# Optimization experiments

Hardware: AMD Instinct MI355X
Metric: run time of the kernel (lower is better)

## Reference

```python
import jax, jax.numpy as jnp
import numpy as np

N, E, IN_C, HID_C, OUT_C = 50000, 800000, 64, 64, 8
NEG_SLOPE = 0.2


def setup_inputs() -> dict:
    key = jax.random.key(0)
    ks = jax.random.split(key, 12)
    return {
        "x": jax.random.normal(ks[0], (N, IN_C), dtype=jnp.float32),
        "edge_index": jax.random.randint(ks[1], (2, E), 0, N, dtype=jnp.int64),
        "edge_value": jax.random.uniform(ks[2], (E,), dtype=jnp.float32),
        "W1": jax.random.normal(ks[3], (IN_C, HID_C), dtype=jnp.float32) * 0.1,
        "a1_src": jax.random.normal(ks[4], (HID_C,), dtype=jnp.float32) * 0.1,
        "a1_dst": jax.random.normal(ks[5], (HID_C,), dtype=jnp.float32) * 0.1,
        "b1": jnp.zeros((HID_C,), dtype=jnp.float32),
        "W2": jax.random.normal(ks[6], (HID_C, OUT_C), dtype=jnp.float32) * 0.1,
        "a2_src": jax.random.normal(ks[7], (OUT_C,), dtype=jnp.float32) * 0.1,
        "a2_dst": jax.random.normal(ks[8], (OUT_C,), dtype=jnp.float32) * 0.1,
        "b2": jnp.zeros((OUT_C,), dtype=jnp.float32),
    }


def _rgat_conv(x, src, dst, edge_value, W, a_src, a_dst, b, n_nodes):
    # Linear transform: [N, out_c]
    h = x @ W
    # Per-node attention halves, gathered per edge -> per-edge logit
    e_src = h @ a_src  # [N]
    e_dst = h @ a_dst  # [N]
    logits = jax.nn.leaky_relu(e_src[src] + e_dst[dst], negative_slope=NEG_SLOPE)  # [E]
    # Segment softmax over destination neighborhoods (numerically stable)
    m = jax.ops.segment_max(logits, dst, num_segments=n_nodes)  # [N]
    ex = jnp.exp(logits - m[dst])
    denom = jax.ops.segment_sum(ex, dst, num_segments=n_nodes)  # [N]
    alpha = ex / (denom[dst] + 1e-16)  # [E]
    # Edge-weighted messages, scatter-aggregate to destinations
    msg = (alpha * edge_value)[:, None] * h[src]  # [E, out_c]
    out = jax.ops.segment_sum(msg, dst, num_segments=n_nodes)  # [N, out_c]
    return out + b


def reference(x, edge_index, edge_value, W1, a1_src, a1_dst, b1, W2, a2_src, a2_dst, b2):
    src, dst = edge_index[0], edge_index[1]
    n = x.shape[0]
    hid = _rgat_conv(x, src, dst, edge_value, W1, a1_src, a1_dst, b1, n)
    hid = jax.nn.relu(hid)
    out = _rgat_conv(hid, src, dst, edge_value, W2, a2_src, a2_dst, b2, n)
    return jax.nn.log_softmax(out, axis=1)
```

## Files before the change

### kernel.cpp

```cpp
#include <hip/hip_runtime.h>
#include <hip/hip_fp16.h>
#include <math.h>


#define CHUNK 4096
#define NBKT  256
#define CAP   6144
#define NPW   4

typedef unsigned long long ull;
typedef float v2f __attribute__((ext_vector_type(2)));

struct PartSmem {
    int lhist[NBKT], lbase[NBKT], lcur[NBKT], gbase[NBKT];
    ull buf[CHUNK];
};
struct GemmSmem {
    float4 Wl[64 * 16];
    float  Xt[64 * 64];
};
union FusedSmem { PartSmem p; GemmSmem g; };


__global__ void __launch_bounds__(256) part_gemm_kernel(
    const int* __restrict__ src, const int* __restrict__ dst,
    const float* __restrict__ ev, int* __restrict__ bcnt,
    ull* __restrict__ ped, int E, int nchunks,
    const float* __restrict__ x, const float* __restrict__ W,
    const float* __restrict__ a_src, const float* __restrict__ a_dst,
    unsigned* __restrict__ h, float* __restrict__ es, float* __restrict__ ed,
    int N)
{
    __shared__ FusedSmem sm;
    const int t = threadIdx.x;

    if (blockIdx.x < nchunks) {
        int e0 = blockIdx.x * CHUNK;
        int cnt = min(CHUNK, E - e0);
        sm.p.lhist[t] = 0;
        __syncthreads();
        for (int i = t; i < cnt; i += 256)
            atomicAdd(&sm.p.lhist[dst[e0 + i] >> 8], 1);
        __syncthreads();
        int myc = sm.p.lhist[t];
        sm.p.lbase[t] = myc;
        __syncthreads();
        for (int o = 1; o < 256; o <<= 1) {
            int add = (t >= o) ? sm.p.lbase[t - o] : 0;
            __syncthreads();
            sm.p.lbase[t] += add;
            __syncthreads();
        }
        int excl = sm.p.lbase[t] - myc;
        sm.p.gbase[t] = myc ? atomicAdd(&bcnt[t], myc) : 0;
        __syncthreads();
        sm.p.lbase[t] = excl;
        sm.p.lcur[t] = excl;
        __syncthreads();
        for (int i = t; i < cnt; i += 256) {
            int e = e0 + i;
            int d = dst[e];
            int b = d >> 8;
            unsigned p = (unsigned)src[e] | ((unsigned)(d & 255) << 16)
                       | ((unsigned)b << 24);
            ull q = (ull)p | ((ull)__float_as_uint(ev[e]) << 32);
            int r = atomicAdd(&sm.p.lcur[b], 1);
            sm.p.buf[r] = q;
        }
        __syncthreads();
        for (int i = t; i < cnt; i += 256) {
            ull q = sm.p.buf[i];
            int b = (int)((q >> 24) & 255);
            ped[(size_t)b * CAP + sm.p.gbase[b] + i - sm.p.lbase[b]] = q;
        }
        return;
    }

    const int n0 = (blockIdx.x - nchunks) * 64;

    #pragma unroll
    for (int i = 0; i < 4; ++i)
        sm.g.Wl[t + i * 256] = ((const float4*)W)[t + i * 256];

    #pragma unroll
    for (int i = 0; i < 4; ++i) {
        int f   = t + i * 256;
        int row = f >> 4, kq = f & 15;
        int grow = n0 + row;
        float4 v = make_float4(0.f, 0.f, 0.f, 0.f);
        if (grow < N) v = ((const float4*)x)[(size_t)grow * 16 + kq];
        int rs = row ^ ((kq & 3) << 2);
        sm.g.Xt[(kq * 4 + 0) * 64 + rs] = v.x;
        sm.g.Xt[(kq * 4 + 1) * 64 + rs] = v.y;
        sm.g.Xt[(kq * 4 + 2) * 64 + rs] = v.z;
        sm.g.Xt[(kq * 4 + 3) * 64 + rs] = v.w;
    }

    const int tx = t & 15;
    const int ty = t >> 4;
    const float4 asv = ((const float4*)a_src)[tx];
    const float4 adv = ((const float4*)a_dst)[tx];
    __syncthreads();

    float4 acc0 = make_float4(0.f,0.f,0.f,0.f);
    float4 acc1 = make_float4(0.f,0.f,0.f,0.f);
    float4 acc2 = make_float4(0.f,0.f,0.f,0.f);
    float4 acc3 = make_float4(0.f,0.f,0.f,0.f);

    #pragma unroll 8
    for (int k = 0; k < 64; ++k) {
        int swz = (k >> 2) & 3;
        const float4 xr = *(const float4*)&sm.g.Xt[k * 64 + ((ty ^ swz) << 2)];
        const float4 wv = sm.g.Wl[k * 16 + tx];
        acc0.x += xr.x * wv.x; acc0.y += xr.x * wv.y;
        acc0.z += xr.x * wv.z; acc0.w += xr.x * wv.w;
        acc1.x += xr.y * wv.x; acc1.y += xr.y * wv.y;
        acc1.z += xr.y * wv.z; acc1.w += xr.y * wv.w;
        acc2.x += xr.z * wv.x; acc2.y += xr.z * wv.y;
        acc2.z += xr.z * wv.z; acc2.w += xr.z * wv.w;
        acc3.x += xr.w * wv.x; acc3.y += xr.w * wv.y;
        acc3.z += xr.w * wv.z; acc3.w += xr.w * wv.w;
    }

    float4 accs[4] = {acc0, acc1, acc2, acc3};
    #pragma unroll
    for (int r = 0; r < 4; ++r) {
        int grow = n0 + ty * 4 + r;
        float4 a = accs[r];
        if (grow < N) {
            int lo = __builtin_amdgcn_cvt_pk_fp8_f32(a.x, a.y, 0, false);
            int pk = __builtin_amdgcn_cvt_pk_fp8_f32(a.z, a.w, lo, true);
            h[(size_t)grow * 16 + tx] = (unsigned)pk;
        }
        float ps = a.x * asv.x + a.y * asv.y + a.z * asv.z + a.w * asv.w;
        float pd = a.x * adv.x + a.y * adv.y + a.z * adv.z + a.w * adv.w;
        #pragma unroll
        for (int o = 8; o > 0; o >>= 1) {
            ps += __shfl_xor(ps, o);
            pd += __shfl_xor(pd, o);
        }
        if (tx == 0 && grow < N) { es[grow] = ps; ed[grow] = pd; }
    }
}


__global__ void __launch_bounds__(1024) csr2_kernel(
    const ull* __restrict__ ped, const int* __restrict__ bcnt,
    int* __restrict__ off, int* __restrict__ deg,
    ull* __restrict__ csre, int N)
{
    __shared__ int cl[256], sc[256], cur[256];
    int b = blockIdx.x, t = threadIdx.x;
    const int cnt = min(bcnt[b], CAP);
    const size_t base = (size_t)b * CAP;
    if (t < 256) cl[t] = 0;
    __syncthreads();
    for (int i = t; i < cnt; i += 1024)
        atomicAdd(&cl[(int)((ped[base + i] >> 16) & 255)], 1);
    __syncthreads();
    int myc = (t < 256) ? cl[t] : 0;
    if (t < 256) sc[t] = myc;
    __syncthreads();
    for (int o = 1; o < 256; o <<= 1) {
        int add = (t >= o && t < 256) ? sc[t - o] : 0;
        __syncthreads();
        if (t < 256) sc[t] += add;
        __syncthreads();
    }
    if (t < 256) {
        int excl = sc[t] - myc;
        int node = b * 256 + t;
        if (node < N) { off[node] = (int)base + excl; deg[node] = myc; }
        cur[t] = excl;
    }
    __syncthreads();
    for (int i = t; i < cnt; i += 1024) {
        ull q = ped[base + i];
        int dloc = (int)((q >> 16) & 255);
        int pos = (int)base + atomicAdd(&cur[dloc], 1);
        csre[pos] = (q & 0xFFFFFFFF00000000ull) | (q & 0xFFFFull);
    }
}


__global__ void __launch_bounds__(256) agg64_fused_kernel(
    const int* __restrict__ off, const int* __restrict__ deg,
    const ull* __restrict__ csre,
    const float* __restrict__ es, const float* __restrict__ ed,
    const unsigned* __restrict__ h, const float* __restrict__ b1,
    const float* __restrict__ W2, const float* __restrict__ a2s,
    const float* __restrict__ a2d, float* __restrict__ h2,
    float* __restrict__ es2, float* __restrict__ ed2, int N)
{
    const int wid = threadIdx.x >> 6, lane = threadIdx.x & 63;
    const int g  = lane >> 4;
    const int c4 = lane & 15;
    const int n0 = (blockIdx.x * 4 + wid) * NPW;
    if (n0 >= N) return;
    const int n1 = min(n0 + NPW, N);

    const int c0 = 2 * g, c1 = 2 * g + 1;
    float w2r0[4], w2r1[4];
    #pragma unroll
    for (int j = 0; j < 4; ++j) {
        w2r0[j] = W2[(4 * c4 + j) * 8 + c0];
        w2r1[j] = W2[(4 * c4 + j) * 8 + c1];
    }
    const float4 b1v = *(const float4*)&b1[c4 << 2];
    const float a2sv0 = a2s[c0], a2sv1 = a2s[c1];
    const float a2dv0 = a2d[c0], a2dv1 = a2d[c1];

    int offv = 0, degv = 0;
    float edv = 0.f;
    {
        int nn = n0 + (lane & (NPW - 1));
        if (nn < N) { offv = off[nn]; degv = deg[nn]; edv = ed[nn]; }
    }

    int svS; float evS, esS;
    unsigned pu0, pu1, pu2, pu3;
    {
        int begX = __shfl(offv, 0);
        int cntX = min(__shfl(degv, 0), 64);
        int idxX = begX + min(lane, max(cntX, 1) - 1);
        ull recX = csre[idxX];
        svS = (int)(recX & 0xFFFFull);
        evS = __uint_as_float((unsigned)(recX >> 32));
        esS = es[svS];
        int s0 = __shfl(svS, g),     s1 = __shfl(svS, 4 + g);
        int s2 = __shfl(svS, 8 + g), s3 = __shfl(svS, 12 + g);
        pu0 = h[(size_t)s0 * 16 + c4];
        pu1 = h[(size_t)s1 * 16 + c4];
        pu2 = h[(size_t)s2 * 16 + c4];
        pu3 = h[(size_t)s3 * 16 + c4];
    }

    for (int n = n0; n < n1; ++n) {
        const int nl = n - n0;
        const int beg = __shfl(offv, nl);
        const int dg  = __shfl(degv, nl);
        const float edn = __shfl(edv, nl);
        const int cnt0 = min(dg, 64);

        const int   sv = svS;
        float z = esS + edn;
        float l = z > 0.f ? z : 0.2f * z;
        float q = (lane < cnt0) ? __expf(l) : 0.f;
        float den = q;
        const float wv = q * evS;

        const unsigned cu0 = pu0, cu1 = pu1, cu2 = pu2, cu3 = pu3;

        if (n + 1 < n1) {
            int begX = __shfl(offv, nl + 1);
            int cntX = min(__shfl(degv, nl + 1), 64);
            int idxX = begX + min(lane, max(cntX, 1) - 1);
            ull recX = csre[idxX];
            svS = (int)(recX & 0xFFFFull);
            evS = __uint_as_float((unsigned)(recX >> 32));
            esS = es[svS];
            int s0 = __shfl(svS, g),     s1 = __shfl(svS, 4 + g);
            int s2 = __shfl(svS, 8 + g), s3 = __shfl(svS, 12 + g);
            pu0 = h[(size_t)s0 * 16 + c4];
            pu1 = h[(size_t)s1 * 16 + c4];
            pu2 = h[(size_t)s2 * 16 + c4];
            pu3 = h[(size_t)s3 * 16 + c4];
        }

        float4 acc = make_float4(0.f, 0.f, 0.f, 0.f);
        {
            float w0 = __shfl(wv, g),     w1 = __shfl(wv, 4 + g);
            float w2 = __shfl(wv, 8 + g), w3 = __shfl(wv, 12 + g);
            v2f f0a = __builtin_amdgcn_cvt_pk_f32_fp8((int)cu0, false);
            v2f f0b = __builtin_amdgcn_cvt_pk_f32_fp8((int)cu0, true);
            v2f f1a = __builtin_amdgcn_cvt_pk_f32_fp8((int)cu1, false);
            v2f f1b = __builtin_amdgcn_cvt_pk_f32_fp8((int)cu1, true);
            v2f f2a = __builtin_amdgcn_cvt_pk_f32_fp8((int)cu2, false);
            v2f f2b = __builtin_amdgcn_cvt_pk_f32_fp8((int)cu2, true);
            v2f f3a = __builtin_amdgcn_cvt_pk_f32_fp8((int)cu3, false);
            v2f f3b = __builtin_amdgcn_cvt_pk_f32_fp8((int)cu3, true);
            acc.x += w0 * f0a.x + w1 * f1a.x + w2 * f2a.x + w3 * f3a.x;
            acc.y += w0 * f0a.y + w1 * f1a.y + w2 * f2a.y + w3 * f3a.y;
            acc.z += w0 * f0b.x + w1 * f1b.x + w2 * f2b.x + w3 * f3b.x;
            acc.w += w0 * f0b.y + w1 * f1b.y + w2 * f2b.y + w3 * f3b.y;
        }
        for (int j = 16; j < cnt0; j += 16) {
            int j0 = j + g, j1 = j + 4 + g, j2 = j + 8 + g, j3 = j + 12 + g;
            int   s0 = __shfl(sv, j0), s1 = __shfl(sv, j1);
            int   s2 = __shfl(sv, j2), s3 = __shfl(sv, j3);
            float w0 = __shfl(wv, j0), w1 = __shfl(wv, j1);
            float w2 = __shfl(wv, j2), w3 = __shfl(wv, j3);
            const unsigned u0 = h[(size_t)s0 * 16 + c4];
            const unsigned u1 = h[(size_t)s1 * 16 + c4];
            const unsigned u2 = h[(size_t)s2 * 16 + c4];
            const unsigned u3 = h[(size_t)s3 * 16 + c4];
            v2f f0a = __builtin_amdgcn_cvt_pk_f32_fp8((int)u0, false);
            v2f f0b = __builtin_amdgcn_cvt_pk_f32_fp8((int)u0, true);
            v2f f1a = __builtin_amdgcn_cvt_pk_f32_fp8((int)u1, false);
            v2f f1b = __builtin_amdgcn_cvt_pk_f32_fp8((int)u1, true);
            v2f f2a = __builtin_amdgcn_cvt_pk_f32_fp8((int)u2, false);
            v2f f2b = __builtin_amdgcn_cvt_pk_f32_fp8((int)u2, true);
            v2f f3a = __builtin_amdgcn_cvt_pk_f32_fp8((int)u3, false);
            v2f f3b = __builtin_amdgcn_cvt_pk_f32_fp8((int)u3, true);
            acc.x += w0 * f0a.x + w1 * f1a.x + w2 * f2a.x + w3 * f3a.x;
            acc.y += w0 * f0a.y + w1 * f1a.y + w2 * f2a.y + w3 * f3a.y;
            acc.z += w0 * f0b.x + w1 * f1b.x + w2 * f2b.x + w3 * f3b.x;
            acc.w += w0 * f0b.y + w1 * f1b.y + w2 * f2b.y + w3 * f3b.y;
        }
        for (int base = beg + 64; base < beg + dg; base += 64) {
            const int cnt = min(beg + dg - base, 64);
            const int idx = base + min(lane, cnt - 1);
            const ull rec = csre[idx];
            const int sv2 = (int)(rec & 0xFFFFull);
            const float ev2 = __uint_as_float((unsigned)(rec >> 32));
            float z2 = es[sv2] + edn;
            float l2 = z2 > 0.f ? z2 : 0.2f * z2;
            float q2 = (lane < cnt) ? __expf(l2) : 0.f;
            den += q2;
            const float wv2 = q2 * ev2;
            for (int j = 0; j < cnt; j += 16) {
                int j0 = j + g, j1 = j + 4 + g, j2 = j + 8 + g, j3 = j + 12 + g;
                int   s0 = __shfl(sv2, j0), s1 = __shfl(sv2, j1);
                int   s2 = __shfl(sv2, j2), s3 = __shfl(sv2, j3);
                float w0 = __shfl(wv2, j0), w1 = __shfl(wv2, j1);
                float w2 = __shfl(wv2, j2), w3 = __shfl(wv2, j3);
                const unsigned u0 = h[(size_t)s0 * 16 + c4];
                const unsigned u1 = h[(size_t)s1 * 16 + c4];
                const unsigned u2 = h[(size_t)s2 * 16 + c4];
                const unsigned u3 = h[(size_t)s3 * 16 + c4];
                v2f f0a = __builtin_amdgcn_cvt_pk_f32_fp8((int)u0, false);
                v2f f0b = __builtin_amdgcn_cvt_pk_f32_fp8((int)u0, true);
                v2f f1a = __builtin_amdgcn_cvt_pk_f32_fp8((int)u1, false);
                v2f f1b = __builtin_amdgcn_cvt_pk_f32_fp8((int)u1, true);
                v2f f2a = __builtin_amdgcn_cvt_pk_f32_fp8((int)u2, false);
                v2f f2b = __builtin_amdgcn_cvt_pk_f32_fp8((int)u2, true);
                v2f f3a = __builtin_amdgcn_cvt_pk_f32_fp8((int)u3, false);
                v2f f3b = __builtin_amdgcn_cvt_pk_f32_fp8((int)u3, true);
                acc.x += w0 * f0a.x + w1 * f1a.x + w2 * f2a.x + w3 * f3a.x;
                acc.y += w0 * f0a.y + w1 * f1a.y + w2 * f2a.y + w3 * f3a.y;
                acc.z += w0 * f0b.x + w1 * f1b.x + w2 * f2b.x + w3 * f3b.x;
                acc.w += w0 * f0b.y + w1 * f1b.y + w2 * f2b.y + w3 * f3b.y;
            }
        }

        #pragma unroll
        for (int o = 16; o < 64; o <<= 1) {
            acc.x += __shfl_xor(acc.x, o);
            acc.y += __shfl_xor(acc.y, o);
            acc.z += __shfl_xor(acc.z, o);
            acc.w += __shfl_xor(acc.w, o);
        }
        #pragma unroll
        for (int o = 1; o < 64; o <<= 1) den += __shfl_xor(den, o);

        const float inv = 1.f / (den + 1e-16f);
        float4 hid;
        hid.x = fmaxf(acc.x * inv + b1v.x, 0.f);
        hid.y = fmaxf(acc.y * inv + b1v.y, 0.f);
        hid.z = fmaxf(acc.z * inv + b1v.z, 0.f);
        hid.w = fmaxf(acc.w * inv + b1v.w, 0.f);

        float p0 = hid.x * w2r0[0] + hid.y * w2r0[1] + hid.z * w2r0[2] + hid.w * w2r0[3];
        float p1 = hid.x * w2r1[0] + hid.y * w2r1[1] + hid.z * w2r1[2] + hid.w * w2r1[3];
        #pragma unroll
        for (int o = 1; o < 16; o <<= 1) {
            p0 += __shfl_xor(p0, o);
            p1 += __shfl_xor(p1, o);
        }
        float psv = p0 * a2sv0 + p1 * a2sv1;
        float pdv = p0 * a2dv0 + p1 * a2dv1;
        #pragma unroll
        for (int o = 16; o < 64; o <<= 1) {
            psv += __shfl_xor(psv, o);
            pdv += __shfl_xor(pdv, o);
        }
        if (c4 == 0)
            *(float2*)&h2[(size_t)n * 8 + c0] = make_float2(p0, p1);
        if (lane == 0) { es2[n] = psv; ed2[n] = pdv; }
    }
}


__global__ void __launch_bounds__(256) agg8_lsm_kernel(
    const int* __restrict__ off, const int* __restrict__ deg,
    const ull* __restrict__ csre,
    const float* __restrict__ es, const float* __restrict__ ed,
    const float* __restrict__ h2, const float* __restrict__ b,
    float* __restrict__ out, int N)
{
    const int wid = threadIdx.x >> 6, lane = threadIdx.x & 63;
    const int g  = lane >> 2;
    const int cp = lane & 3;
    const int n0 = (blockIdx.x * 4 + wid) * NPW;
    if (n0 >= N) return;
    const int n1 = min(n0 + NPW, N);
    const float bc0 = b[2 * cp], bc1 = b[2 * cp + 1];

    int offv = 0, degv = 0;
    float edv = 0.f;
    {
        int nn = n0 + (lane & (NPW - 1));
        if (nn < N) { offv = off[nn]; degv = deg[nn]; edv = ed[nn]; }
    }

    int svS; float evS, esS;
    float2 pf0, pf1;
    {
        int begX = __shfl(offv, 0);
        int cntX = min(__shfl(degv, 0), 64);
        int idxX = begX + min(lane, max(cntX, 1) - 1);
        ull recX = csre[idxX];
        svS = (int)(recX & 0xFFFFull);
        evS = __uint_as_float((unsigned)(recX >> 32));
        esS = es[svS];
        int s0 = __shfl(svS, g), s1 = __shfl(svS, 16 + g);
        pf0 = *(const float2*)&h2[(size_t)s0 * 8 + 2 * cp];
        pf1 = *(const float2*)&h2[(size_t)s1 * 8 + 2 * cp];
    }

    for (int n = n0; n < n1; ++n) {
        const int nl = n - n0;
        const int beg = __shfl(offv, nl);
        const int dg  = __shfl(degv, nl);
        const float edn = __shfl(edv, nl);
        const int cnt0 = min(dg, 64);

        const int   sv = svS;
        float z = esS + edn;
        float l = z > 0.f ? z : 0.2f * z;
        float q = (lane < cnt0) ? __expf(l) : 0.f;
        float den = q;
        const float wv = q * evS;

        const float2 cf0 = pf0, cf1 = pf1;

        if (n + 1 < n1) {
            int begX = __shfl(offv, nl + 1);
            int cntX = min(__shfl(degv, nl + 1), 64);
            int idxX = begX + min(lane, max(cntX, 1) - 1);
            ull recX = csre[idxX];
            svS = (int)(recX & 0xFFFFull);
            evS = __uint_as_float((unsigned)(recX >> 32));
            esS = es[svS];
            int s0 = __shfl(svS, g), s1 = __shfl(svS, 16 + g);
            pf0 = *(const float2*)&h2[(size_t)s0 * 8 + 2 * cp];
            pf1 = *(const float2*)&h2[(size_t)s1 * 8 + 2 * cp];
        }

        float a0, a1;
        {
            float w0 = __shfl(wv, g), w1 = __shfl(wv, 16 + g);
            a0 = w0 * cf0.x + w1 * cf1.x;
            a1 = w0 * cf0.y + w1 * cf1.y;
        }
        for (int j = 32; j < cnt0; j += 32) {
            int j0 = j + g, j1 = j + 16 + g;
            int   s0 = __shfl(sv, j0), s1 = __shfl(sv, j1);
            float w0 = __shfl(wv, j0), w1 = __shfl(wv, j1);
            const float2 f0 = *(const float2*)&h2[(size_t)s0 * 8 + 2 * cp];
            const float2 f1 = *(const float2*)&h2[(size_t)s1 * 8 + 2 * cp];
            a0 += w0 * f0.x + w1 * f1.x;
            a1 += w0 * f0.y + w1 * f1.y;
        }
        for (int base = beg + 64; base < beg + dg; base += 64) {
            const int cnt = min(beg + dg - base, 64);
            const int idx = base + min(lane, cnt - 1);
            const ull rec = csre[idx];
            const int sv2 = (int)(rec & 0xFFFFull);
            const float ev2 = __uint_as_float((unsigned)(rec >> 32));
            float z2 = es[sv2] + edn;
            float l2 = z2 > 0.f ? z2 : 0.2f * z2;
            float q2 = (lane < cnt) ? __expf(l2) : 0.f;
            den += q2;
            const float wv2 = q2 * ev2;
            for (int j = 0; j < cnt; j += 32) {
                int j0 = j + g, j1 = j + 16 + g;
                int   s0 = __shfl(sv2, j0), s1 = __shfl(sv2, j1);
                float w0 = __shfl(wv2, j0), w1 = __shfl(wv2, j1);
                const float2 f0 = *(const float2*)&h2[(size_t)s0 * 8 + 2 * cp];
                const float2 f1 = *(const float2*)&h2[(size_t)s1 * 8 + 2 * cp];
                a0 += w0 * f0.x + w1 * f1.x;
                a1 += w0 * f0.y + w1 * f1.y;
            }
        }

        #pragma unroll
        for (int o = 4; o < 64; o <<= 1) {
            a0 += __shfl_xor(a0, o);
            a1 += __shfl_xor(a1, o);
        }
        #pragma unroll
        for (int o = 1; o < 64; o <<= 1) den += __shfl_xor(den, o);

        const float inv = 1.f / (den + 1e-16f);
        float v0 = a0 * inv + bc0;
        float v1 = a1 * inv + bc1;
        float vm = fmaxf(v0, v1);
        vm = fmaxf(vm, __shfl_xor(vm, 1));
        vm = fmaxf(vm, __shfl_xor(vm, 2));
        float s = __expf(v0 - vm) + __expf(v1 - vm);
        s += __shfl_xor(s, 1);
        s += __shfl_xor(s, 2);
        float lse = vm + logf(s);
        if (lane < 4)
            *(float2*)&out[(size_t)n * 8 + 2 * cp] = make_float2(v0 - lse, v1 - lse);
    }
}


extern "C" void kernel_launch(void* const* d_in, const int* in_sizes, int n_in,
                              void* d_out, int out_size, void* d_ws, size_t ws_size,
                              hipStream_t stream)
{
    const float* x   = (const float*)d_in[0];
    const int*   ei  = (const int*)d_in[1];
    const float* ev  = (const float*)d_in[2];
    const float* W1  = (const float*)d_in[3];
    const float* a1s = (const float*)d_in[4];
    const float* a1d = (const float*)d_in[5];
    const float* b1  = (const float*)d_in[6];
    const float* W2  = (const float*)d_in[7];
    const float* a2s = (const float*)d_in[8];
    const float* a2d = (const float*)d_in[9];
    const float* b2  = (const float*)d_in[10];
    float* out = (float*)d_out;

    const int N = in_sizes[0] / 64;
    const int E = in_sizes[2];
    const int* srcp = ei;
    const int* dstp = ei + E;
    const int nchunks = (E + CHUNK - 1) / CHUNK;
    const int ngemm   = (N + 63) / 64;
    const int nbuck = (N + 255) / 256;
    const int nodes_per_block = 4 * NPW;

    ull*   ped  = (ull*)d_ws;
    ull*   csre = ped + (size_t)NBKT * CAP;
    int*   bcnt = (int*)(csre + (size_t)NBKT * CAP);
    int*   off  = bcnt + NBKT;
    int*   deg  = off + N;
    float* es1  = (float*)(deg + N);
    float* ed1  = es1 + N;
    float* es2  = ed1 + N;
    float* ed2  = es2 + N;
    unsigned* h1 = (unsigned*)(ed2 + N);
    float* h2   = (float*)(h1 + (size_t)N * 16);

    hipMemsetAsync(bcnt, 0, NBKT * sizeof(int), stream);

    part_gemm_kernel<<<nchunks + ngemm, 256, 0, stream>>>(
        srcp, dstp, ev, bcnt, ped, E, nchunks,
        x, W1, a1s, a1d, h1, es1, ed1, N);

    csr2_kernel<<<nbuck, 1024, 0, stream>>>(ped, bcnt, off, deg, csre, N);

    agg64_fused_kernel<<<(N + nodes_per_block - 1) / nodes_per_block, 256, 0, stream>>>(
        off, deg, csre, es1, ed1, h1, b1, W2, a2s, a2d, h2, es2, ed2, N);

    agg8_lsm_kernel<<<(N + nodes_per_block - 1) / nodes_per_block, 256, 0, stream>>>(
        off, deg, csre, es2, ed2, h2, b2, out, N);
}
```

Measured before the change: 157.1 us.

## Widen per-lane gathers and use transpose-reduce butterflies in aggregation kernels

Both aggregation kernels now assign fewer edges per lane group but load wider vectors per lane (uint4 of fp8 in layer one, float4 in layer two), so each lane issues one wide gather per edge instead of several narrow ones. Cross-lane reduction switches to a halving transpose-reduce butterfly, where lanes exchange half their partial vector at each step and end up owning a single channel. The fused W2 projection and the log-softmax are reworked around that per-lane channel ownership. This cuts the number of memory instructions and shuffles, at the cost of more accumulator registers (16 floats per lane in layer one) and more select logic in the reductions.

New measurement: 156.6 us. No clear change (-0.3%).

```diff
diff --git a/kernel.cpp b/kernel.cpp
--- a/kernel.cpp
+++ b/kernel.cpp
@@ -183,6 +183,26 @@
 }
 
 
+#define UNPACK_ACC16(u, we)                                              \
+    do {                                                                 \
+        v2f f0a = __builtin_amdgcn_cvt_pk_f32_fp8((int)(u).x, false);    \
+        v2f f0b = __builtin_amdgcn_cvt_pk_f32_fp8((int)(u).x, true);     \
+        v2f f1a = __builtin_amdgcn_cvt_pk_f32_fp8((int)(u).y, false);    \
+        v2f f1b = __builtin_amdgcn_cvt_pk_f32_fp8((int)(u).y, true);     \
+        v2f f2a = __builtin_amdgcn_cvt_pk_f32_fp8((int)(u).z, false);    \
+        v2f f2b = __builtin_amdgcn_cvt_pk_f32_fp8((int)(u).z, true);     \
+        v2f f3a = __builtin_amdgcn_cvt_pk_f32_fp8((int)(u).w, false);    \
+        v2f f3b = __builtin_amdgcn_cvt_pk_f32_fp8((int)(u).w, true);     \
+        acc[0]  += (we) * f0a.x;  acc[1]  += (we) * f0a.y;               \
+        acc[2]  += (we) * f0b.x;  acc[3]  += (we) * f0b.y;               \
+        acc[4]  += (we) * f1a.x;  acc[5]  += (we) * f1a.y;               \
+        acc[6]  += (we) * f1b.x;  acc[7]  += (we) * f1b.y;               \
+        acc[8]  += (we) * f2a.x;  acc[9]  += (we) * f2a.y;               \
+        acc[10] += (we) * f2b.x;  acc[11] += (we) * f2b.y;               \
+        acc[12] += (we) * f3a.x;  acc[13] += (we) * f3a.y;               \
+        acc[14] += (we) * f3b.x;  acc[15] += (we) * f3b.y;               \
+    } while (0)
+
 __global__ void __launch_bounds__(256) agg64_fused_kernel(
     const int* __restrict__ off, const int* __restrict__ deg,
     const ull* __restrict__ csre,
@@ -193,22 +213,24 @@
     float* __restrict__ es2, float* __restrict__ ed2, int N)
 {
     const int wid = threadIdx.x >> 6, lane = threadIdx.x & 63;
-    const int g  = lane >> 4;
-    const int c4 = lane & 15;
+    const int eslot = lane >> 2;
+    const int q     = lane & 3;
     const int n0 = (blockIdx.x * 4 + wid) * NPW;
     if (n0 >= N) return;
     const int n1 = min(n0 + NPW, N);
 
-    const int c0 = 2 * g, c1 = 2 * g + 1;
-    float w2r0[4], w2r1[4];
-    #pragma unroll
-    for (int j = 0; j < 4; ++j) {
-        w2r0[j] = W2[(4 * c4 + j) * 8 + c0];
-        w2r1[j] = W2[(4 * c4 + j) * 8 + c1];
-    }
-    const float4 b1v = *(const float4*)&b1[c4 << 2];
-    const float a2sv0 = a2s[c0], a2sv1 = a2s[c1];
-    const float a2dv0 = a2d[c0], a2dv1 = a2d[c1];
+    const int ch = 16 * q + 8 * ((lane >> 2) & 1) + 4 * ((lane >> 3) & 1)
+                 + 2 * ((lane >> 4) & 1) + ((lane >> 5) & 1);
+    const float b1c = b1[ch];
+    float w2row[8];
+    {
+        const float4 wa = ((const float4*)(W2 + ch * 8))[0];
+        const float4 wb = ((const float4*)(W2 + ch * 8))[1];
+        w2row[0] = wa.x; w2row[1] = wa.y; w2row[2] = wa.z; w2row[3] = wa.w;
+        w2row[4] = wb.x; w2row[5] = wb.y; w2row[6] = wb.z; w2row[7] = wb.w;
+    }
+    const int olane = 4 * (lane & 1) + 2 * ((lane >> 1) & 1) + ((lane >> 2) & 1);
+    const float a2sv = a2s[olane], a2dv = a2d[olane];
 
     int offv = 0, degv = 0;
     float edv = 0.f;
@@ -218,7 +240,7 @@
     }
 
     int svS; float evS, esS;
-    unsigned pu0, pu1, pu2, pu3;
+    uint4 puS;
     {
         int begX = __shfl(offv, 0);
         int cntX = min(__shfl(degv, 0), 64);
@@ -227,12 +249,8 @@
         svS = (int)(recX & 0xFFFFull);
         evS = __uint_as_float((unsigned)(recX >> 32));
         esS = es[svS];
-        int s0 = __shfl(svS, g),     s1 = __shfl(svS, 4 + g);
-        int s2 = __shfl(svS, 8 + g), s3 = __shfl(svS, 12 + g);
-        pu0 = h[(size_t)s0 * 16 + c4];
-        pu1 = h[(size_t)s1 * 16 + c4];
-        pu2 = h[(size_t)s2 * 16 + c4];
-        pu3 = h[(size_t)s3 * 16 + c4];
+        int s0 = __shfl(svS, eslot);
+        puS = *(const uint4*)&h[(size_t)s0 * 16 + q * 4];
     }
 
     for (int n = n0; n < n1; ++n) {
@@ -242,14 +260,14 @@
         const float edn = __shfl(edv, nl);
         const int cnt0 = min(dg, 64);
 
-        const int   sv = svS;
+        const int sv = svS;
         float z = esS + edn;
         float l = z > 0.f ? z : 0.2f * z;
-        float q = (lane < cnt0) ? __expf(l) : 0.f;
-        float den = q;
-        const float wv = q * evS;
-
-        const unsigned cu0 = pu0, cu1 = pu1, cu2 = pu2, cu3 = pu3;
+        float qv = (lane < cnt0) ? __expf(l) : 0.f;
+        float den = qv;
+        const float wv = qv * evS;
+
+        const uint4 cu = puS;
 
         if (n + 1 < n1) {
             int begX = __shfl(offv, nl + 1);
@@ -259,57 +277,27 @@
             svS = (int)(recX & 0xFFFFull);
             evS = __uint_as_float((unsigned)(recX >> 32));
             esS = es[svS];
-            int s0 = __shfl(svS, g),     s1 = __shfl(svS, 4 + g);
-            int s2 = __shfl(svS, 8 + g), s3 = __shfl(svS, 12 + g);
-            pu0 = h[(size_t)s0 * 16 + c4];
-            pu1 = h[(size_t)s1 * 16 + c4];
-            pu2 = h[(size_t)s2 * 16 + c4];
-            pu3 = h[(size_t)s3 * 16 + c4];
-        }
-
-        float4 acc = make_float4(0.f, 0.f, 0.f, 0.f);
-        {
-            float w0 = __shfl(wv, g),     w1 = __shfl(wv, 4 + g);
-            float w2 = __shfl(wv, 8 + g), w3 = __shfl(wv, 12 + g);
-            v2f f0a = __builtin_amdgcn_cvt_pk_f32_fp8((int)cu0, false);
-            v2f f0b = __builtin_amdgcn_cvt_pk_f32_fp8((int)cu0, true);
-            v2f f1a = __builtin_amdgcn_cvt_pk_f32_fp8((int)cu1, false);
-            v2f f1b = __builtin_amdgcn_cvt_pk_f32_fp8((int)cu1, true);
-            v2f f2a = __builtin_amdgcn_cvt_pk_f32_fp8((int)cu2, false);
-            v2f f2b = __builtin_amdgcn_cvt_pk_f32_fp8((int)cu2, true);
-            v2f f3a = __builtin_amdgcn_cvt_pk_f32_fp8((int)cu3, false);
-            v2f f3b = __builtin_amdgcn_cvt_pk_f32_fp8((int)cu3, true);
-            acc.x += w0 * f0a.x + w1 * f1a.x + w2 * f2a.x + w3 * f3a.x;
-            acc.y += w0 * f0a.y + w1 * f1a.y + w2 * f2a.y + w3 * f3a.y;
-            acc.z += w0 * f0b.x + w1 * f1b.x + w2 * f2b.x + w3 * f3b.x;
-            acc.w += w0 * f0b.y + w1 * f1b.y + w2 * f2b.y + w3 * f3b.y;
+            int s0 = __shfl(svS, eslot);
+            puS = *(const uint4*)&h[(size_t)s0 * 16 + q * 4];
+        }
+
+        float acc[16];
+        #pragma unroll
+        for (int k = 0; k < 16; ++k) acc[k] = 0.f;
+
+        {
+            float we = __shfl(wv, eslot);
+            UNPACK_ACC16(cu, we);
         }
         for (int j = 16; j < cnt0; j += 16) {
-            int j0 = j + g, j1 = j + 4 + g, j2 = j + 8 + g, j3 = j + 12 + g;
-            int   s0 = __shfl(sv, j0), s1 = __shfl(sv, j1);
-            int   s2 = __shfl(sv, j2), s3 = __shfl(sv, j3);
-            float w0 = __shfl(wv, j0), w1 = __shfl(wv, j1);
-            float w2 = __shfl(wv, j2), w3 = __shfl(wv, j3);
-            const unsigned u0 = h[(size_t)s0 * 16 + c4];
-            const unsigned u1 = h[(size_t)s1 * 16 + c4];
-            const unsigned u2 = h[(size_t)s2 * 16 + c4];
-            const unsigned u3 = h[(size_t)s3 * 16 + c4];
-            v2f f0a = __builtin_amdgcn_cvt_pk_f32_fp8((int)u0, false);
-            v2f f0b = __builtin_amdgcn_cvt_pk_f32_fp8((int)u0, true);
-            v2f f1a = __builtin_amdgcn_cvt_pk_f32_fp8((int)u1, false);
-            v2f f1b = __builtin_amdgcn_cvt_pk_f32_fp8((int)u1, true);
-            v2f f2a = __builtin_amdgcn_cvt_pk_f32_fp8((int)u2, false);
-            v2f f2b = __builtin_amdgcn_cvt_pk_f32_fp8((int)u2, true);
-            v2f f3a = __builtin_amdgcn_cvt_pk_f32_fp8((int)u3, false);
-            v2f f3b = __builtin_amdgcn_cvt_pk_f32_fp8((int)u3, true);
-            acc.x += w0 * f0a.x + w1 * f1a.x + w2 * f2a.x + w3 * f3a.x;
-            acc.y += w0 * f0a.y + w1 * f1a.y + w2 * f2a.y + w3 * f3a.y;
-            acc.z += w0 * f0b.x + w1 * f1b.x + w2 * f2b.x + w3 * f3b.x;
-            acc.w += w0 * f0b.y + w1 * f1b.y + w2 * f2b.y + w3 * f3b.y;
-        }
-        for (int base = beg + 64; base < beg + dg; base += 64) {
-            const int cnt = min(beg + dg - base, 64);
-            const int idx = base + min(lane, cnt - 1);
+            int   se = __shfl(sv, j + eslot);
+            float we = __shfl(wv, j + eslot);
+            const uint4 u = *(const uint4*)&h[(size_t)se * 16 + q * 4];
+            UNPACK_ACC16(u, we);
+        }
+        for (int base2 = beg + 64; base2 < beg + dg; base2 += 64) {
+            const int cnt = min(beg + dg - base2, 64);
+            const int idx = base2 + min(lane, cnt - 1);
             const ull rec = csre[idx];
             const int sv2 = (int)(rec & 0xFFFFull);
             const float ev2 = __uint_as_float((unsigned)(rec >> 32));
@@ -319,64 +307,101 @@
             den += q2;
             const float wv2 = q2 * ev2;
             for (int j = 0; j < cnt; j += 16) {
-                int j0 = j + g, j1 = j + 4 + g, j2 = j + 8 + g, j3 = j + 12 + g;
-                int   s0 = __shfl(sv2, j0), s1 = __shfl(sv2, j1);
-                int   s2 = __shfl(sv2, j2), s3 = __shfl(sv2, j3);
-                float w0 = __shfl(wv2, j0), w1 = __shfl(wv2, j1);
-                float w2 = __shfl(wv2, j2), w3 = __shfl(wv2, j3);
-                const unsigned u0 = h[(size_t)s0 * 16 + c4];
-                const unsigned u1 = h[(size_t)s1 * 16 + c4];
-                const unsigned u2 = h[(size_t)s2 * 16 + c4];
-                const unsigned u3 = h[(size_t)s3 * 16 + c4];
-                v2f f0a = __builtin_amdgcn_cvt_pk_f32_fp8((int)u0, false);
-                v2f f0b = __builtin_amdgcn_cvt_pk_f32_fp8((int)u0, true);
-                v2f f1a = __builtin_amdgcn_cvt_pk_f32_fp8((int)u1, false);
-                v2f f1b = __builtin_amdgcn_cvt_pk_f32_fp8((int)u1, true);
-                v2f f2a = __builtin_amdgcn_cvt_pk_f32_fp8((int)u2, false);
-                v2f f2b = __builtin_amdgcn_cvt_pk_f32_fp8((int)u2, true);
-                v2f f3a = __builtin_amdgcn_cvt_pk_f32_fp8((int)u3, false);
-                v2f f3b = __builtin_amdgcn_cvt_pk_f32_fp8((int)u3, true);
-                acc.x += w0 * f0a.x + w1 * f1a.x + w2 * f2a.x + w3 * f3a.x;
-                acc.y += w0 * f0a.y + w1 * f1a.y + w2 * f2a.y + w3 * f3a.y;
-                acc.z += w0 * f0b.x + w1 * f1b.x + w2 * f2b.x + w3 * f3b.x;
-                acc.w += w0 * f0b.y + w1 * f1b.y + w2 * f2b.y + w3 * f3b.y;
-            }
-        }
-
+                int   se = __shfl(sv2, j + eslot);
+                float we = __shfl(wv2, j + eslot);
+                const uint4 u = *(const uint4*)&h[(size_t)se * 16 + q * 4];
+                UNPACK_ACC16(u, we);
+            }
+        }
+
+        float r8[8];
+        {
+            const bool hi = (lane & 4);
+            #pragma unroll
+            for (int k = 0; k < 8; ++k) {
+                float keep = hi ? acc[k + 8] : acc[k];
+                float send = hi ? acc[k]     : acc[k + 8];
+                r8[k] = keep + __shfl_xor(send, 4);
+            }
+            den += __shfl_xor(den, 4);
+        }
+        float r4[4];
+        {
+            const bool hi = (lane & 8);
+            #pragma unroll
+            for (int k = 0; k < 4; ++k) {
+                float keep = hi ? r8[k + 4] : r8[k];
+                float send = hi ? r8[k]     : r8[k + 4];
+                r4[k] = keep + __shfl_xor(send, 8);
+            }
+            den += __shfl_xor(den, 8);
+        }
+        float r2[2];
+        {
+            const bool hi = (lane & 16);
+            #pragma unroll
+            for (int k = 0; k < 2; ++k) {
+                float keep = hi ? r4[k + 2] : r4[k];
+                float send = hi ? r4[k]     : r4[k + 2];
+                r2[k] = keep + __shfl_xor(send, 16);
+            }
+            den += __shfl_xor(den, 16);
+        }
+        float r1;
+        {
+            const bool hi = (lane & 32);
+            float keep = hi ? r2[1] : r2[0];
+            float send = hi ? r2[0] : r2[1];
+            r1 = keep + __shfl_xor(send, 32);
+            den += __shfl_xor(den, 32);
+        }
+        den += __shfl_xor(den, 1);
+        den += __shfl_xor(den, 2);
+
+        const float inv = 1.f / (den + 1e-16f);
+        const float hid = fmaxf(r1 * inv + b1c, 0.f);
+
+        float p[8];
         #pragma unroll
-        for (int o = 16; o < 64; o <<= 1) {
-            acc.x += __shfl_xor(acc.x, o);
-            acc.y += __shfl_xor(acc.y, o);
-            acc.z += __shfl_xor(acc.z, o);
-            acc.w += __shfl_xor(acc.w, o);
-        }
-        #pragma unroll
-        for (int o = 1; o < 64; o <<= 1) den += __shfl_xor(den, o);
-
-        const float inv = 1.f / (den + 1e-16f);
-        float4 hid;
-        hid.x = fmaxf(acc.x * inv + b1v.x, 0.f);
-        hid.y = fmaxf(acc.y * inv + b1v.y, 0.f);
-        hid.z = fmaxf(acc.z * inv + b1v.z, 0.f);
-        hid.w = fmaxf(acc.w * inv + b1v.w, 0.f);
-
-        float p0 = hid.x * w2r0[0] + hid.y * w2r0[1] + hid.z * w2r0[2] + hid.w * w2r0[3];
-        float p1 = hid.x * w2r1[0] + hid.y * w2r1[1] + hid.z * w2r1[2] + hid.w * w2r1[3];
-        #pragma unroll
-        for (int o = 1; o < 16; o <<= 1) {
-            p0 += __shfl_xor(p0, o);
-            p1 += __shfl_xor(p1, o);
-        }
-        float psv = p0 * a2sv0 + p1 * a2sv1;
-        float pdv = p0 * a2dv0 + p1 * a2dv1;
-        #pragma unroll
-        for (int o = 16; o < 64; o <<= 1) {
-            psv += __shfl_xor(psv, o);
-            pdv += __shfl_xor(pdv, o);
-        }
-        if (c4 == 0)
-            *(float2*)&h2[(size_t)n * 8 + c0] = make_float2(p0, p1);
-        if (lane == 0) { es2[n] = psv; ed2[n] = pdv; }
+        for (int k = 0; k < 8; ++k) p[k] = hid * w2row[k];
+        float s4[4];
+        {
+            const bool hi = (lane & 1);
+            #pragma unroll
+            for (int k = 0; k < 4; ++k) {
+                float keep = hi ? p[k + 4] : p[k];
+                float send = hi ? p[k]     : p[k + 4];
+                s4[k] = keep + __shfl_xor(send, 1);
+            }
+        }
+        float s2[2];
+        {
+            const bool hi = (lane & 2);
+            #pragma unroll
+            for (int k = 0; k < 2; ++k) {
+                float keep = hi ? s4[k + 2] : s4[k];
+                float send = hi ? s4[k]     : s4[k + 2];
+                s2[k] = keep + __shfl_xor(send, 2);
+            }
+        }
+        float s1;
+        {
+            const bool hi = (lane & 4);
+            float keep = hi ? s2[1] : s2[0];
+            float send = hi ? s2[0] : s2[1];
+            s1 = keep + __shfl_xor(send, 4);
+        }
+        s1 += __shfl_xor(s1, 8);
+        s1 += __shfl_xor(s1, 16);
+        s1 += __shfl_xor(s1, 32);
+
+        float ts = s1 * a2sv, td = s1 * a2dv;
+        ts += __shfl_xor(ts, 1); td += __shfl_xor(td, 1);
+        ts += __shfl_xor(ts, 2); td += __shfl_xor(td, 2);
+        ts += __shfl_xor(ts, 4); td += __shfl_xor(td, 4);
+
+        if (lane < 8) h2[(size_t)n * 8 + olane] = s1;
+        if (lane == 0) { es2[n] = ts; ed2[n] = td; }
     }
 }
 
@@ -389,12 +414,14 @@
     float* __restrict__ out, int N)
 {
     const int wid = threadIdx.x >> 6, lane = threadIdx.x & 63;
-    const int g  = lane >> 2;
-    const int cp = lane & 3;
+    const int eslot = lane >> 1;
+    const int hh = lane & 1;
     const int n0 = (blockIdx.x * 4 + wid) * NPW;
     if (n0 >= N) return;
     const int n1 = min(n0 + NPW, N);
-    const float bc0 = b[2 * cp], bc1 = b[2 * cp + 1];
+
+    const int ch = 4 * (lane & 1) + 2 * ((lane >> 1) & 1) + ((lane >> 2) & 1);
+    const float bc = b[ch];
 
     int offv = 0, degv = 0;
     float edv = 0.f;
@@ -404,7 +431,7 @@
     }
 
     int svS; float evS, esS;
-    float2 pf0, pf1;
+    float4 pf;
     {
         int begX = __shfl(offv, 0);
         int cntX = min(__shfl(degv, 0), 64);
@@ -413,9 +440,8 @@
         svS = (int)(recX & 0xFFFFull);
         evS = __uint_as_float((unsigned)(recX >> 32));
         esS = es[svS];
-        int s0 = __shfl(svS, g), s1 = __shfl(svS, 16 + g);
-        pf0 = *(const float2*)&h2[(size_t)s0 * 8 + 2 * cp];
-        pf1 = *(const float2*)&h2[(size_t)s1 * 8 + 2 * cp];
+        int s0 = __shfl(svS, eslot);
+        pf = *(const float4*)&h2[(size_t)s0 * 8 + 4 * hh];
     }
 
     for (int n = n0; n < n1; ++n) {
@@ -425,14 +451,14 @@
         const float edn = __shfl(edv, nl);
         const int cnt0 = min(dg, 64);
 
-        const int   sv = svS;
+        const int sv = svS;
         float z = esS + edn;
         float l = z > 0.f ? z : 0.2f * z;
-        float q = (lane < cnt0) ? __expf(l) : 0.f;
-        float den = q;
-        const float wv = q * evS;
-
-        const float2 cf0 = pf0, cf1 = pf1;
+        float qv = (lane < cnt0) ? __expf(l) : 0.f;
+        float den = qv;
+        const float wv = qv * evS;
+
+        const float4 cf = pf;
 
         if (n + 1 < n1) {
             int begX = __shfl(offv, nl + 1);
@@ -442,29 +468,26 @@
             svS = (int)(recX & 0xFFFFull);
             evS = __uint_as_float((unsigned)(recX >> 32));
             esS = es[svS];
-            int s0 = __shfl(svS, g), s1 = __shfl(svS, 16 + g);
-            pf0 = *(const float2*)&h2[(size_t)s0 * 8 + 2 * cp];
-            pf1 = *(const float2*)&h2[(size_t)s1 * 8 + 2 * cp];
-        }
-
-        float a0, a1;
-        {
-            float w0 = __shfl(wv, g), w1 = __shfl(wv, 16 + g);
-            a0 = w0 * cf0.x + w1 * cf1.x;
-            a1 = w0 * cf0.y + w1 * cf1.y;
+            int s0 = __shfl(svS, eslot);
+            pf = *(const float4*)&h2[(size_t)s0 * 8 + 4 * hh];
+        }
+
+        float acc[4];
+        {
+            float we = __shfl(wv, eslot);
+            acc[0] = we * cf.x; acc[1] = we * cf.y;
+            acc[2] = we * cf.z; acc[3] = we * cf.w;
         }
         for (int j = 32; j < cnt0; j += 32) {
-            int j0 = j + g, j1 = j + 16 + g;
-            int   s0 = __shfl(sv, j0), s1 = __shfl(sv, j1);
-            float w0 = __shfl(wv, j0), w1 = __shfl(wv, j1);
-            const float2 f0 = *(const float2*)&h2[(size_t)s0 * 8 + 2 * cp];
-            const float2 f1 = *(const float2*)&h2[(size_t)s1 * 8 + 2 * cp];
-            a0 += w0 * f0.x + w1 * f1.x;
-            a1 += w0 * f0.y + w1 * f1.y;
-        }
-        for (int base = beg + 64; base < beg + dg; base += 64) {
-            const int cnt = min(beg + dg - base, 64);
-            const int idx = base + min(lane, cnt - 1);
+            int   se = __shfl(sv, j + eslot);
+            float we = __shfl(wv, j + eslot);
+            const float4 f = *(const float4*)&h2[(size_t)se * 8 + 4 * hh];
+            acc[0] += we * f.x; acc[1] += we * f.y;
+            acc[2] += we * f.z; acc[3] += we * f.w;
+        }
+        for (int base2 = beg + 64; base2 < beg + dg; base2 += 64) {
+            const int cnt = min(beg + dg - base2, 64);
+            const int idx = base2 + min(lane, cnt - 1);
             const ull rec = csre[idx];
             const int sv2 = (int)(rec & 0xFFFFull);
             const float ev2 = __uint_as_float((unsigned)(rec >> 32));
@@ -474,36 +497,52 @@
             den += q2;
             const float wv2 = q2 * ev2;
             for (int j = 0; j < cnt; j += 32) {
-                int j0 = j + g, j1 = j + 16 + g;
-                int   s0 = __shfl(sv2, j0), s1 = __shfl(sv2, j1);
-                float w0 = __shfl(wv2, j0), w1 = __shfl(wv2, j1);
-                const float2 f0 = *(const float2*)&h2[(size_t)s0 * 8 + 2 * cp];
-                const float2 f1 = *(const float2*)&h2[(size_t)s1 * 8 + 2 * cp];
-                a0 += w0 * f0.x + w1 * f1.x;
-                a1 += w0 * f0.y + w1 * f1.y;
-            }
-        }
-
-        #pragma unroll
-        for (int o = 4; o < 64; o <<= 1) {
-            a0 += __shfl_xor(a0, o);
-            a1 += __shfl_xor(a1, o);
-        }
-        #pragma unroll
-        for (int o = 1; o < 64; o <<= 1) den += __shfl_xor(den, o);
+                int   se = __shfl(sv2, j + eslot);
+                float we = __shfl(wv2, j + eslot);
+                const float4 f = *(const float4*)&h2[(size_t)se * 8 + 4 * hh];
+                acc[0] += we * f.x; acc[1] += we * f.y;
+                acc[2] += we * f.z; acc[3] += we * f.w;
+            }
+        }
+
+        float r2[2];
+        {
+            const bool hi = (lane & 2);
+            #pragma unroll
+            for (int k = 0; k < 2; ++k) {
+                float keep = hi ? acc[k + 2] : acc[k];
+                float send = hi ? acc[k]     : acc[k + 2];
+                r2[k] = keep + __shfl_xor(send, 2);
+            }
+            den += __shfl_xor(den, 2);
+        }
+        float r1;
+        {
+            const bool hi = (lane & 4);
+            float keep = hi ? r2[1] : r2[0];
+            float send = hi ? r2[0] : r2[1];
+            r1 = keep + __shfl_xor(send, 4);
+            den += __shfl_xor(den, 4);
+        }
+        r1 += __shfl_xor(r1, 8);   den += __shfl_xor(den, 8);
+        r1 += __shfl_xor(r1, 16);  den += __shfl_xor(den, 16);
+        r1 += __shfl_xor(r1, 32);  den += __shfl_xor(den, 32);
+        den += __shfl_xor(den, 1);
 
         const float inv = 1.f / (den + 1e-16f);
-        float v0 = a0 * inv + bc0;
-        float v1 = a1 * inv + bc1;
-        float vm = fmaxf(v0, v1);
+        const float v = r1 * inv + bc;
+
+        float vm = v;
         vm = fmaxf(vm, __shfl_xor(vm, 1));
         vm = fmaxf(vm, __shfl_xor(vm, 2));
-        float s = __expf(v0 - vm) + __expf(v1 - vm);
+        vm = fmaxf(vm, __shfl_xor(vm, 4));
+        float s = __expf(v - vm);
         s += __shfl_xor(s, 1);
         s += __shfl_xor(s, 2);
+        s += __shfl_xor(s, 4);
         float lse = vm + logf(s);
-        if (lane < 4)
-            *(float2*)&out[(size_t)n * 8 + 2 * cp] = make_float2(v0 - lse, v1 - lse);
+        if (lane < 8)
+            out[(size_t)n * 8 + ch] = v - lse;
     }
 }
 
```
